# Kernel optimization log

Measured on AMD Instinct MI355X. Metric: run time of the kernel, lower is better.

## Reference

```python
import jax, jax.numpy as jnp
import numpy as np

DIM = 1024
NUM_HEADS = 16
HEAD_DIM = DIM // NUM_HEADS
SCALE = HEAD_DIM ** -0.5


def setup_inputs() -> dict:
    key = jax.random.key(0)
    k_x, k_qkv, k_pw, k_pb = jax.random.split(key, 4)
    B, L = 2, 2048
    x = jax.random.normal(k_x, (B, L, DIM), dtype=jnp.float32)
    # nn.Linear weights are [out, in]; stored the same way here.
    w_qkv = jax.random.normal(k_qkv, (3 * DIM, DIM), dtype=jnp.float32) * (DIM ** -0.5)
    w_proj = jax.random.normal(k_pw, (DIM, DIM), dtype=jnp.float32) * (DIM ** -0.5)
    b_proj = jax.random.normal(k_pb, (DIM,), dtype=jnp.float32) * 0.01
    return {"x": x, "w_qkv": w_qkv, "w_proj": w_proj, "b_proj": b_proj}


def reference(x, w_qkv, w_proj, b_proj):
    B, L, P = x.shape
    H, D = NUM_HEADS, HEAD_DIM
    # qkv projection (no bias): [B, L, 3*P]
    qkv = jnp.einsum('blp,op->blo', x, w_qkv)
    qkv = qkv.reshape(B, L, 3, H, D).transpose(2, 0, 3, 1, 4)  # [3, B, H, L, D]
    q, k, v = qkv[0], qkv[1], qkv[2]
    attn = jnp.einsum('bhld,bhmd->bhlm', q, k) * SCALE  # [B, H, L, L]
    attn = jax.nn.softmax(attn, axis=-1)
    out = jnp.einsum('bhlm,bhmd->bhld', attn, v)  # [B, H, L, D]
    out = out.transpose(0, 2, 1, 3).reshape(B, L, P)
    out = jnp.einsum('blp,op->blo', out, w_proj) + b_proj
    return out
```

## Files before the change

kernel.cpp:

```cpp
#include <hip/hip_runtime.h>
#include <hip/hip_bf16.h>
#include <stdint.h>
#include <stddef.h>

typedef short s16x8 __attribute__((ext_vector_type(8)));
typedef float f32x4  __attribute__((ext_vector_type(4)));
typedef float f32x16 __attribute__((ext_vector_type(16)));
typedef unsigned int u32x2 __attribute__((ext_vector_type(2)));

#define MFMA16(a, b, c) __builtin_amdgcn_mfma_f32_16x16x32_bf16((a), (b), (c), 0, 0, 0)
#define MFMA32(a, b, c) __builtin_amdgcn_mfma_f32_32x32x16_bf16((a), (b), (c), 0, 0, 0)
#define EXP2(x) __builtin_amdgcn_exp2f(x)

__device__ __forceinline__ unsigned short f2bf(float f) {
  union { float f; uint32_t u; } v; v.f = f;
  uint32_t u = v.u;
  return (unsigned short)((u + 0x7FFFu + ((u >> 16) & 1u)) >> 16);
}

__device__ __forceinline__ unsigned int pack_bf16x2(float a, float b) {
  __hip_bfloat162 h = __float22bfloat162_rn(make_float2(a, b));
  union { __hip_bfloat162 h; unsigned int u; } c; c.h = h;
  return c.u;
}

__device__ __forceinline__ void load_lds16(const void* gsrc, void* ldst) {
  void* gp = const_cast<void*>(gsrc);
  __builtin_amdgcn_global_load_lds(
      (__attribute__((address_space(1))) void*)gp,
      (__attribute__((address_space(3))) void*)ldst, 16, 0, 0);
}

#define B_    2
#define L_    2048
#define DIM_  1024
#define NH_   16
#define HD_   64
#define MTOT  (B_ * L_)
#define QSCALE_ 0.18033688011112042f
#define SMSHIFT_ 16.0f

__global__ void cvt_all(const float* __restrict__ x, const float* __restrict__ wq,
                        const float* __restrict__ wp,
                        unsigned short* __restrict__ xb, unsigned short* __restrict__ wqb,
                        unsigned short* __restrict__ wpb) {
  const int X4 = 1048576, Q4 = 786432;
  int i = blockIdx.x * 256 + threadIdx.x;
  const float* in; unsigned short* out; int idx;
  if (i < X4)            { in = x;  out = xb;  idx = i; }
  else if (i < X4 + Q4)  { in = wq; out = wqb; idx = i - X4; }
  else                   { in = wp; out = wpb; idx = i - X4 - Q4; }
  float4 v = ((const float4*)in)[idx];
  uint2 r;
  r.x = pack_bf16x2(v.x, v.y);
  r.y = pack_bf16x2(v.z, v.w);
  ((uint2*)out)[idx] = r;
}

template <int EPI>
__global__ void __launch_bounds__(256)
gemm_bt(const unsigned short* __restrict__ A,
        const unsigned short* __restrict__ Bw,
        int M, int N, int K,
        unsigned short* __restrict__ Qb,
        unsigned short* __restrict__ Kb,
        unsigned short* __restrict__ Vt,
        float* __restrict__ Cout,
        const float* __restrict__ bias) {
  __shared__ __attribute__((aligned(16))) unsigned short Al[2][128 * 32];
  __shared__ __attribute__((aligned(16))) unsigned short Bl[2][128 * 32];
  const int tid  = threadIdx.x;
  const int lane = tid & 63, wv = tid >> 6;
  const int g = lane >> 4, lr = lane & 15;
  const int wr = wv >> 1, wc = wv & 1;
  const int m0 = blockIdx.x * 128, n0 = blockIdx.y * 128;

  f32x4 acc[4][4];
  const f32x4 zero = {0.f, 0.f, 0.f, 0.f};
#pragma unroll
  for (int i = 0; i < 4; i++)
#pragma unroll
    for (int j = 0; j < 4; j++) acc[i][j] = zero;

#define STAGE_G(buf, k0)                                                              \
  {                                                                                   \
    _Pragma("unroll")                                                                 \
    for (int pass = 0; pass < 2; ++pass) {                                            \
      int c   = pass * 256 + wv * 64 + lane;                                          \
      int row = c >> 2, kc = c & 3;                                                   \
      int ks  = (kc ^ ((row ^ (row >> 2)) & 3)) * 8;                                  \
      load_lds16(A  + (size_t)(m0 + row) * K + (k0) + ks, (char*)&Al[buf][0] + c * 16); \
      load_lds16(Bw + (size_t)(n0 + row) * K + (k0) + ks, (char*)&Bl[buf][0] + c * 16); \
    }                                                                                 \
  }

  STAGE_G(0, 0);
  __syncthreads();
  const int NTk = K >> 5;
  for (int t = 0; t < NTk; ++t) {
    const int cur = t & 1;
    if (t + 1 < NTk) STAGE_G(cur ^ 1, (t + 1) * 32);

    s16x8 af[4], bf[4];
#pragma unroll
    for (int mi = 0; mi < 4; mi++) {
      int row = wr * 64 + mi * 16 + lr;
      int ch  = g ^ ((row ^ (row >> 2)) & 3);
      af[mi]  = *(const s16x8*)((const char*)&Al[cur][0] + row * 64 + ch * 16);
    }
#pragma unroll
    for (int ni = 0; ni < 4; ni++) {
      int row = wc * 64 + ni * 16 + lr;
      int ch  = g ^ ((row ^ (row >> 2)) & 3);
      bf[ni]  = *(const s16x8*)((const char*)&Bl[cur][0] + row * 64 + ch * 16);
    }
#pragma unroll
    for (int mi = 0; mi < 4; mi++)
#pragma unroll
      for (int ni = 0; ni < 4; ni++)
        acc[mi][ni] = MFMA16(af[mi], bf[ni], acc[mi][ni]);
    __syncthreads();
  }
#undef STAGE_G

  if (EPI == 0) {
#pragma unroll
    for (int mi = 0; mi < 4; mi++)
#pragma unroll
      for (int ni = 0; ni < 4; ni++) {
        int ncol = n0 + wc * 64 + ni * 16 + lr;
        int s = ncol >> 10;
        int h = (ncol >> 6) & 15;
        int d = ncol & 63;
#pragma unroll
        for (int j = 0; j < 4; j++) {
          int m = m0 + wr * 64 + mi * 16 + g * 4 + j;
          int b = m >> 11, l = m & 2047;
          size_t bh = (size_t)(b * NH_ + h);
          if (s == 0)      Qb[(bh * L_ + l) * HD_ + d] = f2bf(acc[mi][ni][j] * QSCALE_);
          else if (s == 1) Kb[(bh * L_ + l) * HD_ + d] = f2bf(acc[mi][ni][j]);
          else             Vt[(bh * HD_ + d) * L_ + l] = f2bf(acc[mi][ni][j]);
        }
      }
  } else {
#pragma unroll
    for (int mi = 0; mi < 4; mi++)
#pragma unroll
      for (int ni = 0; ni < 4; ni++) {
        int ncol = n0 + wc * 64 + ni * 16 + lr;
        float bv = bias[ncol];
#pragma unroll
        for (int j = 0; j < 4; j++) {
          int m = m0 + wr * 64 + mi * 16 + g * 4 + j;
          Cout[(size_t)m * N + ncol] = acc[mi][ni][j] + bv;
        }
      }
  }
}

__global__ void __launch_bounds__(512, 4)
attn_fwd(const unsigned short* __restrict__ Qb,
         const unsigned short* __restrict__ Kb,
         const unsigned short* __restrict__ Vt,
         unsigned short* __restrict__ Ob) {
  __shared__ __attribute__((aligned(16))) unsigned short Kl[2][2][64 * 64];
  __shared__ __attribute__((aligned(16))) unsigned short Vl[2][2][64 * 64];

  const int tid  = threadIdx.x;
  const int lane = tid & 63, w = tid >> 6;
  const int sp = w >> 2, wvl = w & 3;
  const int hi = lane >> 5, lq = lane & 31;
  const int f   = blockIdx.y * 16 + blockIdx.x;
  const int swz = (f & 7) * 64 + (f >> 3);
  const int qt = swz & 15, bh = swz >> 4;

  const unsigned short* Qh = Qb + (size_t)bh * L_ * HD_;
  const unsigned short* Kh = Kb + (size_t)bh * L_ * HD_;
  const unsigned short* Vh = Vt + (size_t)bh * HD_ * L_;
  const int q0 = qt * 128 + wvl * 32;
  const int kvbase = sp * (L_ / 2);

  s16x8 qf[4];
#pragma unroll
  for (int ks = 0; ks < 4; ++ks)
    qf[ks] = *(const s16x8*)(Qh + (size_t)(q0 + lq) * HD_ + ks * 16 + hi * 8);

  f32x16 o0, o1;
#pragma unroll
  for (int r = 0; r < 16; ++r) { o0[r] = 0.f; o1[r] = 0.f; }
  float rsum = 0.f;

#define STAGE(buf, kv0)                                                          \
  {                                                                              \
    _Pragma("unroll")                                                            \
    for (int it = 0; it < 2; ++it) {                                             \
      int c = it * 256 + wvl * 64 + lane;                                        \
      int row = c >> 3, cc = c & 7;                                              \
      int cs = (cc ^ (row & 7)) * 8;                                             \
      load_lds16(Kh + (size_t)((kv0) + row) * HD_ + cs, (char*)&Kl[sp][buf][0] + c * 16); \
      load_lds16(Vh + (size_t)row * L_ + (kv0) + cs,    (char*)&Vl[sp][buf][0] + c * 16); \
    }                                                                            \
  }

  STAGE(0, kvbase);
  __syncthreads();

  const int NT = (L_ / 2) / 64;
  for (int t = 0; t < NT; ++t) {
    const int cur = t & 1;
    if (t + 1 < NT) STAGE(cur ^ 1, kvbase + (t + 1) * 64);

    const unsigned short* KL = &Kl[sp][cur][0];
    const unsigned short* VL = &Vl[sp][cur][0];

    f32x16 s0, s1;
#pragma unroll
    for (int r = 0; r < 16; ++r) { s0[r] = -SMSHIFT_; s1[r] = -SMSHIFT_; }
    __builtin_amdgcn_s_setprio(1);
#pragma unroll
    for (int ks = 0; ks < 4; ++ks) {
      int cc = ((ks << 1) | hi) ^ (lq & 7);
      s16x8 k0 = *(const s16x8*)((const char*)KL + lq * 128 + cc * 16);
      s0 = MFMA32(k0, qf[ks], s0);
      s16x8 k1 = *(const s16x8*)((const char*)KL + (32 + lq) * 128 + cc * 16);
      s1 = MFMA32(k1, qf[ks], s1);
    }
    __builtin_amdgcn_s_setprio(0);

#pragma unroll
    for (int r = 0; r < 16; ++r) { s0[r] = EXP2(s0[r]); s1[r] = EXP2(s1[r]); }

    {
      f32x16 ta;
#pragma unroll
      for (int r = 0; r < 16; ++r) ta[r] = s0[r] + s1[r];
#pragma unroll
      for (int wd = 8; wd >= 1; wd >>= 1)
#pragma unroll
        for (int r = 0; r < 8; ++r) if (r < wd) ta[r] += ta[r + wd];
      rsum += ta[0];
    }

#pragma unroll
    for (int st = 0; st < 2; ++st) {
      unsigned int pd[8];
#pragma unroll
      for (int r2 = 0; r2 < 8; ++r2)
        pd[r2] = st ? pack_bf16x2(s1[2 * r2], s1[2 * r2 + 1])
                    : pack_bf16x2(s0[2 * r2], s0[2 * r2 + 1]);
      __builtin_amdgcn_s_setprio(1);
#pragma unroll
      for (int ksl = 0; ksl < 2; ++ksl) {
        u32x2 e0 = __builtin_amdgcn_permlane32_swap(pd[4 * ksl + 0], pd[4 * ksl + 2], false, false);
        u32x2 e1 = __builtin_amdgcn_permlane32_swap(pd[4 * ksl + 1], pd[4 * ksl + 3], false, false);
        union { unsigned int u[4]; s16x8 v; } pa;
        pa.u[0] = e0[0];
        pa.u[1] = e1[0];
        pa.u[2] = e0[1];
        pa.u[3] = e1[1];
#pragma unroll
        for (int dt = 0; dt < 2; ++dt) {
          int row = dt * 32 + lq;
          int cc = (4 * st + 2 * ksl + hi) ^ (row & 7);
          s16x8 vf = *(const s16x8*)((const char*)VL + row * 128 + cc * 16);
          if (dt == 0) o0 = MFMA32(vf, pa.v, o0);
          else         o1 = MFMA32(vf, pa.v, o1);
        }
      }
      __builtin_amdgcn_s_setprio(0);
    }

    __syncthreads();
  }
#undef STAGE

  {
    union { float f; unsigned u; } ru; ru.f = rsum;
    u32x2 rs = __builtin_amdgcn_permlane32_swap(ru.u, ru.u, false, false);
    union { unsigned u; float f; } r0, r1; r0.u = rs[0]; r1.u = rs[1];
    rsum = r0.f + r1.f;
  }

  float* Osh = (float*)&Kl[0][0][0];
  float* Lsh = (float*)&Vl[0][0][0];
  if (sp == 1) {
#pragma unroll
    for (int r = 0; r < 16; ++r) {
      int d = (r & 3) + 8 * (r >> 2) + 4 * hi;
      Osh[wvl * 2048 + d * 32 + lq]        = o0[r];
      Osh[wvl * 2048 + (d + 32) * 32 + lq] = o1[r];
    }
    if (hi == 0) Lsh[wvl * 32 + lq] = rsum;
  }
  __syncthreads();
  if (sp == 0) {
    const float inv = 1.0f / (rsum + Lsh[wvl * 32 + lq]);
#pragma unroll
    for (int r = 0; r < 16; ++r) {
      int d = (r & 3) + 8 * (r >> 2) + 4 * hi;
      o0[r] = (o0[r] + Osh[wvl * 2048 + d * 32 + lq]) * inv;
      o1[r] = (o1[r] + Osh[wvl * 2048 + (d + 32) * 32 + lq]) * inv;
    }
    const int b = bh >> 4, h = bh & 15;
    const int q = q0 + lq;
    size_t base = ((size_t)(b * L_ + q)) * DIM_ + h * HD_;
#pragma unroll
    for (int dt = 0; dt < 2; ++dt)
#pragma unroll
      for (int r2 = 0; r2 < 8; ++r2) {
        int d = dt * 32 + 8 * (r2 >> 1) + 4 * hi + 2 * (r2 & 1);
        float a = dt ? o1[2 * r2] : o0[2 * r2];
        float c = dt ? o1[2 * r2 + 1] : o0[2 * r2 + 1];
        unsigned int pv = pack_bf16x2(a, c);
        *(unsigned int*)((unsigned short*)Ob + base + d) = pv;
      }
  }
}

extern "C" void kernel_launch(void* const* d_in, const int* in_sizes, int n_in,
                              void* d_out, int out_size, void* d_ws, size_t ws_size,
                              hipStream_t stream) {
  const float* x      = (const float*)d_in[0];
  const float* w_qkv  = (const float*)d_in[1];
  const float* w_proj = (const float*)d_in[2];
  const float* b_proj = (const float*)d_in[3];
  float* out = (float*)d_out;

  const size_t N_X    = (size_t)MTOT * DIM_;
  const size_t N_WQKV = (size_t)3 * DIM_ * DIM_;
  const size_t N_WPRJ = (size_t)DIM_ * DIM_;
  const size_t N_QKV  = (size_t)B_ * NH_ * L_ * HD_;

  unsigned short* xb     = (unsigned short*)d_ws;
  unsigned short* wqkvb  = xb + N_X;
  unsigned short* wprojb = wqkvb + N_WQKV;
  unsigned short* Qb     = wprojb + N_WPRJ;
  unsigned short* Kb     = Qb + N_QKV;
  unsigned short* Vt     = Kb + N_QKV;
  unsigned short* Obuf   = Vt + N_QKV;

  cvt_all<<<8192, 256, 0, stream>>>(x, w_qkv, w_proj, xb, wqkvb, wprojb);

  dim3 g1(MTOT / 128, (3 * DIM_) / 128);
  gemm_bt<0><<<g1, 256, 0, stream>>>(xb, wqkvb, MTOT, 3 * DIM_, DIM_,
                                     Qb, Kb, Vt, nullptr, nullptr);

  dim3 g2(L_ / 128, B_ * NH_);
  attn_fwd<<<g2, 512, 0, stream>>>(Qb, Kb, Vt, Obuf);

  dim3 g3(MTOT / 128, DIM_ / 128);
  gemm_bt<1><<<g3, 256, 0, stream>>>(Obuf, wprojb, MTOT, DIM_, DIM_,
                                     nullptr, nullptr, nullptr, out, b_proj);
}
```

Before: 122.3 us.

## Halve attention KV tile to raise occupancy and split projection GEMM tiles

The attention kernel now processes 32 KV rows per iteration instead of 64. This halves the LDS footprint and the score registers, and the launch bound is raised from 4 to 6 blocks per CU to allow more resident waves. The V tile uses a new 64-byte-row swizzle. The output projection GEMM is split into its own kernel with 128x64 tiles, doubling its grid to fill more CUs. The trade-off is twice as many KV loop iterations and barriers, and possible register spilling under the tighter launch bound.

```diff
diff --git a/kernel.cpp b/kernel.cpp
--- a/kernel.cpp
+++ b/kernel.cpp
@@ -57,16 +57,13 @@
   ((uint2*)out)[idx] = r;
 }
 
-template <int EPI>
 __global__ void __launch_bounds__(256)
-gemm_bt(const unsigned short* __restrict__ A,
-        const unsigned short* __restrict__ Bw,
-        int M, int N, int K,
-        unsigned short* __restrict__ Qb,
-        unsigned short* __restrict__ Kb,
-        unsigned short* __restrict__ Vt,
-        float* __restrict__ Cout,
-        const float* __restrict__ bias) {
+gemm_qkv(const unsigned short* __restrict__ A,
+         const unsigned short* __restrict__ Bw,
+         unsigned short* __restrict__ Qb,
+         unsigned short* __restrict__ Kb,
+         unsigned short* __restrict__ Vt) {
+  const int K = DIM_;
   __shared__ __attribute__((aligned(16))) unsigned short Al[2][128 * 32];
   __shared__ __attribute__((aligned(16))) unsigned short Bl[2][128 * 32];
   const int tid  = threadIdx.x;
@@ -123,48 +120,113 @@
   }
 #undef STAGE_G
 
-  if (EPI == 0) {
+#pragma unroll
+  for (int mi = 0; mi < 4; mi++)
+#pragma unroll
+    for (int ni = 0; ni < 4; ni++) {
+      int ncol = n0 + wc * 64 + ni * 16 + lr;
+      int s = ncol >> 10;
+      int h = (ncol >> 6) & 15;
+      int d = ncol & 63;
+#pragma unroll
+      for (int j = 0; j < 4; j++) {
+        int m = m0 + wr * 64 + mi * 16 + g * 4 + j;
+        int b = m >> 11, l = m & 2047;
+        size_t bh = (size_t)(b * NH_ + h);
+        if (s == 0)      Qb[(bh * L_ + l) * HD_ + d] = f2bf(acc[mi][ni][j] * QSCALE_);
+        else if (s == 1) Kb[(bh * L_ + l) * HD_ + d] = f2bf(acc[mi][ni][j]);
+        else             Vt[(bh * HD_ + d) * L_ + l] = f2bf(acc[mi][ni][j]);
+      }
+    }
+}
+
+__global__ void __launch_bounds__(256)
+gemm_proj(const unsigned short* __restrict__ A,
+          const unsigned short* __restrict__ Bw,
+          float* __restrict__ Cout,
+          const float* __restrict__ bias) {
+  const int K = DIM_, N = DIM_;
+  __shared__ __attribute__((aligned(16))) unsigned short Al[2][128 * 32];
+  __shared__ __attribute__((aligned(16))) unsigned short Bl[2][64 * 32];
+  const int tid  = threadIdx.x;
+  const int lane = tid & 63, wv = tid >> 6;
+  const int g = lane >> 4, lr = lane & 15;
+  const int wr = wv >> 1, wc = wv & 1;
+  const int m0 = blockIdx.x * 128, n0 = blockIdx.y * 64;
+
+  f32x4 acc[4][2];
+  const f32x4 zero = {0.f, 0.f, 0.f, 0.f};
+#pragma unroll
+  for (int i = 0; i < 4; i++) { acc[i][0] = zero; acc[i][1] = zero; }
+
+#define STAGE_P(buf, k0)                                                              \
+  {                                                                                   \
+    _Pragma("unroll")                                                                 \
+    for (int pass = 0; pass < 2; ++pass) {                                            \
+      int c   = pass * 256 + wv * 64 + lane;                                          \
+      int row = c >> 2, kc = c & 3;                                                   \
+      int ks  = (kc ^ ((row ^ (row >> 2)) & 3)) * 8;                                  \
+      load_lds16(A + (size_t)(m0 + row) * K + (k0) + ks, (char*)&Al[buf][0] + c * 16); \
+    }                                                                                 \
+    {                                                                                 \
+      int c   = wv * 64 + lane;                                                       \
+      int row = c >> 2, kc = c & 3;                                                   \
+      int ks  = (kc ^ ((row ^ (row >> 2)) & 3)) * 8;                                  \
+      load_lds16(Bw + (size_t)(n0 + row) * K + (k0) + ks, (char*)&Bl[buf][0] + c * 16); \
+    }                                                                                 \
+  }
+
+  STAGE_P(0, 0);
+  __syncthreads();
+  const int NTk = K >> 5;
+  for (int t = 0; t < NTk; ++t) {
+    const int cur = t & 1;
+    if (t + 1 < NTk) STAGE_P(cur ^ 1, (t + 1) * 32);
+
+    s16x8 af[4], bf[2];
+#pragma unroll
+    for (int mi = 0; mi < 4; mi++) {
+      int row = wr * 64 + mi * 16 + lr;
+      int ch  = g ^ ((row ^ (row >> 2)) & 3);
+      af[mi]  = *(const s16x8*)((const char*)&Al[cur][0] + row * 64 + ch * 16);
+    }
+#pragma unroll
+    for (int ni = 0; ni < 2; ni++) {
+      int row = wc * 32 + ni * 16 + lr;
+      int ch  = g ^ ((row ^ (row >> 2)) & 3);
+      bf[ni]  = *(const s16x8*)((const char*)&Bl[cur][0] + row * 64 + ch * 16);
+    }
 #pragma unroll
     for (int mi = 0; mi < 4; mi++)
 #pragma unroll
-      for (int ni = 0; ni < 4; ni++) {
-        int ncol = n0 + wc * 64 + ni * 16 + lr;
-        int s = ncol >> 10;
-        int h = (ncol >> 6) & 15;
-        int d = ncol & 63;
-#pragma unroll
-        for (int j = 0; j < 4; j++) {
-          int m = m0 + wr * 64 + mi * 16 + g * 4 + j;
-          int b = m >> 11, l = m & 2047;
-          size_t bh = (size_t)(b * NH_ + h);
-          if (s == 0)      Qb[(bh * L_ + l) * HD_ + d] = f2bf(acc[mi][ni][j] * QSCALE_);
-          else if (s == 1) Kb[(bh * L_ + l) * HD_ + d] = f2bf(acc[mi][ni][j]);
-          else             Vt[(bh * HD_ + d) * L_ + l] = f2bf(acc[mi][ni][j]);
-        }
+      for (int ni = 0; ni < 2; ni++)
+        acc[mi][ni] = MFMA16(af[mi], bf[ni], acc[mi][ni]);
+    __syncthreads();
+  }
+#undef STAGE_P
+
+#pragma unroll
+  for (int mi = 0; mi < 4; mi++)
+#pragma unroll
+    for (int ni = 0; ni < 2; ni++) {
+      int ncol = n0 + wc * 32 + ni * 16 + lr;
+      float bv = bias[ncol];
+#pragma unroll
+      for (int j = 0; j < 4; j++) {
+        int m = m0 + wr * 64 + mi * 16 + g * 4 + j;
+        Cout[(size_t)m * N + ncol] = acc[mi][ni][j] + bv;
       }
-  } else {
-#pragma unroll
-    for (int mi = 0; mi < 4; mi++)
-#pragma unroll
-      for (int ni = 0; ni < 4; ni++) {
-        int ncol = n0 + wc * 64 + ni * 16 + lr;
-        float bv = bias[ncol];
-#pragma unroll
-        for (int j = 0; j < 4; j++) {
-          int m = m0 + wr * 64 + mi * 16 + g * 4 + j;
-          Cout[(size_t)m * N + ncol] = acc[mi][ni][j] + bv;
-        }
-      }
-  }
-}
-
-__global__ void __launch_bounds__(512, 4)
+    }
+}
+
+__global__ void __launch_bounds__(512, 6)
 attn_fwd(const unsigned short* __restrict__ Qb,
          const unsigned short* __restrict__ Kb,
          const unsigned short* __restrict__ Vt,
          unsigned short* __restrict__ Ob) {
-  __shared__ __attribute__((aligned(16))) unsigned short Kl[2][2][64 * 64];
-  __shared__ __attribute__((aligned(16))) unsigned short Vl[2][2][64 * 64];
+  __shared__ __attribute__((aligned(16))) char smem[33280];
+#define KBUF(s_, b_) ((unsigned short*)(smem + ((s_) * 2 + (b_)) * 4096))
+#define VBUF(s_, b_) ((unsigned short*)(smem + 16384 + ((s_) * 2 + (b_)) * 4096))
 
   const int tid  = threadIdx.x;
   const int lane = tid & 63, w = tid >> 6;
@@ -190,50 +252,45 @@
   for (int r = 0; r < 16; ++r) { o0[r] = 0.f; o1[r] = 0.f; }
   float rsum = 0.f;
 
-#define STAGE(buf, kv0)                                                          \
-  {                                                                              \
-    _Pragma("unroll")                                                            \
-    for (int it = 0; it < 2; ++it) {                                             \
-      int c = it * 256 + wvl * 64 + lane;                                        \
-      int row = c >> 3, cc = c & 7;                                              \
-      int cs = (cc ^ (row & 7)) * 8;                                             \
-      load_lds16(Kh + (size_t)((kv0) + row) * HD_ + cs, (char*)&Kl[sp][buf][0] + c * 16); \
-      load_lds16(Vh + (size_t)row * L_ + (kv0) + cs,    (char*)&Vl[sp][buf][0] + c * 16); \
-    }                                                                            \
+#define STAGE(buf, kv0)                                                            \
+  {                                                                                \
+    int c = wvl * 64 + lane;                                                       \
+    int krow = c >> 3, kcc = c & 7;                                                \
+    int kcs = (kcc ^ (krow & 7)) * 8;                                              \
+    load_lds16(Kh + (size_t)((kv0) + krow) * HD_ + kcs, KBUF(sp, buf) + c * 8);    \
+    int vrow = c >> 2, vcc = c & 3;                                                \
+    int vcs = (vcc ^ ((vrow ^ (vrow >> 2)) & 3)) * 8;                              \
+    load_lds16(Vh + (size_t)vrow * L_ + (kv0) + vcs, VBUF(sp, buf) + c * 8);       \
   }
 
   STAGE(0, kvbase);
   __syncthreads();
 
-  const int NT = (L_ / 2) / 64;
+  const int NT = (L_ / 2) / 32;
   for (int t = 0; t < NT; ++t) {
     const int cur = t & 1;
-    if (t + 1 < NT) STAGE(cur ^ 1, kvbase + (t + 1) * 64);
-
-    const unsigned short* KL = &Kl[sp][cur][0];
-    const unsigned short* VL = &Vl[sp][cur][0];
-
-    f32x16 s0, s1;
-#pragma unroll
-    for (int r = 0; r < 16; ++r) { s0[r] = -SMSHIFT_; s1[r] = -SMSHIFT_; }
+    if (t + 1 < NT) STAGE(cur ^ 1, kvbase + (t + 1) * 32);
+
+    const unsigned short* KL = KBUF(sp, cur);
+    const unsigned short* VL = VBUF(sp, cur);
+
+    f32x16 s0;
+#pragma unroll
+    for (int r = 0; r < 16; ++r) s0[r] = -SMSHIFT_;
     __builtin_amdgcn_s_setprio(1);
 #pragma unroll
     for (int ks = 0; ks < 4; ++ks) {
       int cc = ((ks << 1) | hi) ^ (lq & 7);
       s16x8 k0 = *(const s16x8*)((const char*)KL + lq * 128 + cc * 16);
       s0 = MFMA32(k0, qf[ks], s0);
-      s16x8 k1 = *(const s16x8*)((const char*)KL + (32 + lq) * 128 + cc * 16);
-      s1 = MFMA32(k1, qf[ks], s1);
     }
     __builtin_amdgcn_s_setprio(0);
 
 #pragma unroll
-    for (int r = 0; r < 16; ++r) { s0[r] = EXP2(s0[r]); s1[r] = EXP2(s1[r]); }
+    for (int r = 0; r < 16; ++r) s0[r] = EXP2(s0[r]);
 
     {
-      f32x16 ta;
-#pragma unroll
-      for (int r = 0; r < 16; ++r) ta[r] = s0[r] + s1[r];
+      f32x16 ta = s0;
 #pragma unroll
       for (int wd = 8; wd >= 1; wd >>= 1)
 #pragma unroll
@@ -241,34 +298,30 @@
       rsum += ta[0];
     }
 
-#pragma unroll
-    for (int st = 0; st < 2; ++st) {
-      unsigned int pd[8];
-#pragma unroll
-      for (int r2 = 0; r2 < 8; ++r2)
-        pd[r2] = st ? pack_bf16x2(s1[2 * r2], s1[2 * r2 + 1])
-                    : pack_bf16x2(s0[2 * r2], s0[2 * r2 + 1]);
-      __builtin_amdgcn_s_setprio(1);
-#pragma unroll
-      for (int ksl = 0; ksl < 2; ++ksl) {
-        u32x2 e0 = __builtin_amdgcn_permlane32_swap(pd[4 * ksl + 0], pd[4 * ksl + 2], false, false);
-        u32x2 e1 = __builtin_amdgcn_permlane32_swap(pd[4 * ksl + 1], pd[4 * ksl + 3], false, false);
-        union { unsigned int u[4]; s16x8 v; } pa;
-        pa.u[0] = e0[0];
-        pa.u[1] = e1[0];
-        pa.u[2] = e0[1];
-        pa.u[3] = e1[1];
-#pragma unroll
-        for (int dt = 0; dt < 2; ++dt) {
-          int row = dt * 32 + lq;
-          int cc = (4 * st + 2 * ksl + hi) ^ (row & 7);
-          s16x8 vf = *(const s16x8*)((const char*)VL + row * 128 + cc * 16);
-          if (dt == 0) o0 = MFMA32(vf, pa.v, o0);
-          else         o1 = MFMA32(vf, pa.v, o1);
-        }
+    unsigned int pd[8];
+#pragma unroll
+    for (int r2 = 0; r2 < 8; ++r2)
+      pd[r2] = pack_bf16x2(s0[2 * r2], s0[2 * r2 + 1]);
+    __builtin_amdgcn_s_setprio(1);
+#pragma unroll
+    for (int ksl = 0; ksl < 2; ++ksl) {
+      u32x2 e0 = __builtin_amdgcn_permlane32_swap(pd[4 * ksl + 0], pd[4 * ksl + 2], false, false);
+      u32x2 e1 = __builtin_amdgcn_permlane32_swap(pd[4 * ksl + 1], pd[4 * ksl + 3], false, false);
+      union { unsigned int u[4]; s16x8 v; } pa;
+      pa.u[0] = e0[0];
+      pa.u[1] = e1[0];
+      pa.u[2] = e0[1];
+      pa.u[3] = e1[1];
+#pragma unroll
+      for (int dt = 0; dt < 2; ++dt) {
+        int row = dt * 32 + lq;
+        int p = (2 * ksl + hi) ^ ((row ^ (row >> 2)) & 3);
+        s16x8 vf = *(const s16x8*)((const char*)VL + row * 64 + p * 16);
+        if (dt == 0) o0 = MFMA32(vf, pa.v, o0);
+        else         o1 = MFMA32(vf, pa.v, o1);
       }
-      __builtin_amdgcn_s_setprio(0);
-    }
+    }
+    __builtin_amdgcn_s_setprio(0);
 
     __syncthreads();
   }
@@ -281,8 +334,8 @@
     rsum = r0.f + r1.f;
   }
 
-  float* Osh = (float*)&Kl[0][0][0];
-  float* Lsh = (float*)&Vl[0][0][0];
+  float* Osh = (float*)smem;
+  float* Lsh = (float*)(smem + 32768);
   if (sp == 1) {
 #pragma unroll
     for (int r = 0; r < 16; ++r) {
@@ -315,6 +368,8 @@
         *(unsigned int*)((unsigned short*)Ob + base + d) = pv;
       }
   }
+#undef KBUF
+#undef VBUF
 }
 
 extern "C" void kernel_launch(void* const* d_in, const int* in_sizes, int n_in,
@@ -342,13 +397,11 @@
   cvt_all<<<8192, 256, 0, stream>>>(x, w_qkv, w_proj, xb, wqkvb, wprojb);
 
   dim3 g1(MTOT / 128, (3 * DIM_) / 128);
-  gemm_bt<0><<<g1, 256, 0, stream>>>(xb, wqkvb, MTOT, 3 * DIM_, DIM_,
-                                     Qb, Kb, Vt, nullptr, nullptr);
+  gemm_qkv<<<g1, 256, 0, stream>>>(xb, wqkvb, Qb, Kb, Vt);
 
   dim3 g2(L_ / 128, B_ * NH_);
   attn_fwd<<<g2, 512, 0, stream>>>(Qb, Kb, Vt, Obuf);
 
-  dim3 g3(MTOT / 128, DIM_ / 128);
-  gemm_bt<1><<<g3, 256, 0, stream>>>(Obuf, wprojb, MTOT, DIM_, DIM_,
-                                     nullptr, nullptr, nullptr, out, b_proj);
-}
+  dim3 g3(MTOT / 128, DIM_ / 64);
+  gemm_proj<<<g3, 256, 0, stream>>>(Obuf, wprojb, out, b_proj);
+}
```

New measurement: 187.6 us. +53.4%, slower.
